# Kernel tuning notes

Measured on AMD Instinct MI355X. Metric: run time of the kernel, lower is better.

## Reference

```python
import jax, jax.numpy as jnp
import numpy as np

H = 4
HD = 32
C = 128
NU = 40000
NI = 40000
E = 200000


def _linear(x, W, b):
    # torch Linear: y = x @ W.T + b, W is [out, in]
    return x @ W.T + b


def _counts_in(query, sorted_keys):
    l = jnp.searchsorted(sorted_keys, query, side='left')
    r = jnp.searchsorted(sorted_keys, query, side='right')
    return (r - l).astype(jnp.float32)


def _segment_softmax(scores, seg, n):
    # scores: [E, H], seg: [E] destination ids
    m = jax.ops.segment_max(scores, seg, num_segments=n)
    m = jnp.where(jnp.isfinite(m), m, 0.0)
    e = jnp.exp(scores - m[seg])
    z = jax.ops.segment_sum(e, seg, num_segments=n)
    return e / z[seg]


def _deg_count(idx, n):
    return jnp.zeros((n,), jnp.float32).at[idx].add(1.0)


def _layernorm(x):
    mu = x.mean(-1, keepdims=True)
    var = ((x - mu) ** 2).mean(-1, keepdims=True)
    return (x - mu) / jnp.sqrt(var + 1e-5)


def _relation(x_src, x_dst, src, dst, t_src, t_dst,
              Wq, bq, Wk, bk, Wv, bv, Wo, bo,
              head_bias, beta, tau_raw, gamma, delta,
              counts, recips, n_dst):
    Q = _linear(x_dst, Wq, bq).reshape(-1, H, HD)
    K = _linear(x_src, Wk, bk).reshape(-1, H, HD)
    V = _linear(x_src, Wv, bv).reshape(-1, H, HD)
    Qe, Ke, Ve = Q[dst], K[src], V[src]                      # [E, H, HD]
    scores = (Qe * Ke).sum(-1) / jnp.sqrt(jnp.float32(HD))   # [E, H]
    scores = scores + head_bias
    dt = jnp.abs(t_dst[dst] - t_src[src]) + 1e-6
    tau = jax.nn.softplus(tau_raw) + 1e-6
    scores = scores + (-jnp.log1p(dt / tau))[:, None] * beta
    scores = scores + jnp.log1p(counts)[:, None] * gamma
    scores = scores + recips[:, None] * delta
    w = _segment_softmax(scores, dst, n_dst)                 # [E, H]
    out_e = (Ve * w[:, :, None]).reshape(-1, C)
    out_e = _linear(out_e, Wo, bo)
    return jnp.zeros((n_dst, C), x_dst.dtype).at[dst].add(out_e)


def setup_inputs() -> dict:
    key = jax.random.key(0)
    ks = jax.random.split(key, 20)
    inp = {
        'x_user': jax.random.normal(ks[0], (NU, C), jnp.float32),
        'x_item': jax.random.normal(ks[1], (NI, C), jnp.float32),
        't_user': jax.random.uniform(ks[2], (NU,), jnp.float32) * 100.0,
        't_item': jax.random.uniform(ks[3], (NI,), jnp.float32) * 100.0,
        'edge_index_ui': jax.random.randint(ks[4], (2, E), 0, NU, jnp.int32),
        'edge_index_iu': jax.random.randint(ks[5], (2, E), 0, NI, jnp.int32),
        'Wq': jax.random.normal(ks[6], (C, C), jnp.float32) * 0.05,
        'bq': jax.random.normal(ks[7], (C,), jnp.float32) * 0.05,
        'Wk': jax.random.normal(ks[8], (C, C), jnp.float32) * 0.05,
        'bk': jax.random.normal(ks[9], (C,), jnp.float32) * 0.05,
        'Wv': jax.random.normal(ks[10], (C, C), jnp.float32) * 0.05,
        'bv': jax.random.normal(ks[11], (C,), jnp.float32) * 0.05,
        'Wo': jax.random.normal(ks[12], (C, C), jnp.float32) * 0.05,
        'bo': jax.random.normal(ks[13], (C,), jnp.float32) * 0.05,
        'rel_head_bias': jax.random.normal(ks[14], (2, H), jnp.float32) * 0.1,
        'time_beta': jax.random.normal(ks[15], (2, H), jnp.float32) * 0.1,
        'time_tau_raw': jax.random.normal(ks[16], (2,), jnp.float32),
        'gamma_multirel': jax.random.normal(ks[17], (2, H), jnp.float32) * 0.1,
        'delta_recip': jax.random.normal(ks[18], (2, H), jnp.float32) * 0.1,
    }
    return inp


def reference(x_user, x_item, t_user, t_item, edge_index_ui, edge_index_iu,
              Wq, bq, Wk, bk, Wv, bv, Wo, bo,
              rel_head_bias, time_beta, time_tau_raw, gamma_multirel, delta_recip):
    su, du = edge_index_ui[0], edge_index_ui[1]   # user -> item
    si, di = edge_index_iu[0], edge_index_iu[1]   # item -> user
    # multirel counts (pair multiplicity - 1) and reciprocity flags, per relation
    pid_ui = su * NI + du            # (user,item) pair ids (fits int32: NU*NI < 2^31)
    pid_iu = si * NU + di            # (item,user) pair ids
    rev_for_ui = di * NI + si        # reversed pairs of iu edges in (user,item) space
    rev_for_iu = du * NU + su        # reversed pairs of ui edges in (item,user) space
    counts_ui = _counts_in(pid_ui, jnp.sort(pid_ui)) - 1.0
    counts_iu = _counts_in(pid_iu, jnp.sort(pid_iu)) - 1.0
    recips_ui = (_counts_in(pid_ui, jnp.sort(rev_for_ui)) > 0).astype(jnp.float32)
    recips_iu = (_counts_in(pid_iu, jnp.sort(rev_for_iu)) > 0).astype(jnp.float32)

    out_item = _relation(x_user, x_item, su, du, t_user, t_item,
                         Wq, bq, Wk, bk, Wv, bv, Wo, bo,
                         rel_head_bias[0], time_beta[0], time_tau_raw[0],
                         gamma_multirel[0], delta_recip[0], counts_ui, recips_ui, NI)
    out_user = _relation(x_item, x_user, si, di, t_item, t_user,
                         Wq, bq, Wk, bk, Wv, bv, Wo, bo,
                         rel_head_bias[1], time_beta[1], time_tau_raw[1],
                         gamma_multirel[1], delta_recip[1], counts_iu, recips_iu, NU)
    # degree centrality bias: total (in + out) degree added to every channel
    deg_user = _deg_count(su, NU) + _deg_count(di, NU)
    deg_item = _deg_count(du, NI) + _deg_count(si, NI)
    out_user = out_user + deg_user[:, None]
    out_item = out_item + deg_item[:, None]
    return _layernorm(out_user + x_user), _layernorm(out_item + x_item)
```

## Files before the change

### kernel.cpp

```cpp
#include <hip/hip_runtime.h>
#include <math.h>

constexpr int kH  = 4;
constexpr int kHD = 32;
constexpr int kC  = 128;
constexpr int kNU = 40000;
constexpr int kNI = 40000;
constexpr int kE  = 200000;
constexpr int kNT = kNU + kNI;
constexpr int kTS = 1 << 19;
constexpr int kTMASK = kTS - 1;
constexpr int kSB = (kNT + 1023) / 1024;
constexpr int kTilesPerSide = kNU / 16;
constexpr int kTiles = kNT / 16;

#define DEV_INLINE __device__ __forceinline__

typedef short bf16x8 __attribute__((ext_vector_type(8)));
typedef float f32x4  __attribute__((ext_vector_type(4)));
typedef uint32_t u32x4 __attribute__((ext_vector_type(4)));

DEV_INLINE int hash_slot(int pid) {
  uint32_t h = (uint32_t)pid * 2654435761u;
  return (int)((h >> 13) & kTMASK);
}

DEV_INLINE unsigned short f2bf(float f) {
  uint32_t u = __float_as_uint(f);
  u += 0x7fffu + ((u >> 16) & 1u);
  return (unsigned short)(u >> 16);
}

DEV_INLINE float bflo(uint32_t u) { return __uint_as_float(u << 16); }
DEV_INLINE float bfhi(uint32_t u) { return __uint_as_float(u & 0xffff0000u); }

DEV_INLINE int swz(int row, int elem) {
  return (elem & 7) | (((elem >> 3) ^ (row & 7)) << 3);
}

__global__ void cast4w_bf16(const float* __restrict__ w0, const float* __restrict__ w1,
                            const float* __restrict__ w2, const float* __restrict__ w3,
                            unsigned short* __restrict__ o0, unsigned short* __restrict__ o1,
                            unsigned short* __restrict__ o2, unsigned short* __restrict__ o3) {
  int i = blockIdx.x * blockDim.x + threadIdx.x;
  int m = i >> 12, j = i & 4095;
  const float* in = (m == 0) ? w0 : (m == 1) ? w1 : (m == 2) ? w2 : w3;
  unsigned short* out = (m == 0) ? o0 : (m == 1) ? o1 : (m == 2) ? o2 : o3;
  float4 v = ((const float4*)in)[j];
  ushort4 o = {f2bf(v.x), f2bf(v.y), f2bf(v.z), f2bf(v.w)};
  ((ushort4*)out)[j] = o;
}

__global__ __launch_bounds__(256, 3) void qkv_ws(
    const float* __restrict__ Xu, const float* __restrict__ Xi,
    const unsigned short* __restrict__ Wq, const unsigned short* __restrict__ Wk,
    const unsigned short* __restrict__ Wv,
    const float* __restrict__ bq, const float* __restrict__ bk,
    const float* __restrict__ bv,
    unsigned short* __restrict__ Qu, unsigned short* __restrict__ Ku,
    unsigned short* __restrict__ Vu,
    unsigned short* __restrict__ Qi, unsigned short* __restrict__ Ki,
    unsigned short* __restrict__ Vi) {
  __shared__ unsigned short sx[16 * kC];
  __shared__ unsigned short sr[3 * 16 * kC];
  const int tid  = threadIdx.x;
  const int wave = tid >> 6;
  const int lane = tid & 63;
  const int mr   = lane & 15;
  const int quad = lane >> 4;
  const int ct0  = wave * 2;
  const int srow = tid >> 4;
  const int schk = tid & 15;

  bf16x8 wf[3][2][4];
  {
    const unsigned short* Ws[3] = {Wq, Wk, Wv};
#pragma unroll
    for (int m = 0; m < 3; ++m)
#pragma unroll
      for (int c = 0; c < 2; ++c) {
        const unsigned short* wrow = Ws[m] + (size_t)((ct0 + c) * 16 + mr) * kC + quad * 8;
#pragma unroll
        for (int kc = 0; kc < 4; ++kc) wf[m][c][kc] = *(const bf16x8*)(wrow + kc * 32);
      }
  }

  int tile = blockIdx.x;
  float4 xa, xb;
  {
    const bool item = tile >= kTilesPerSide;
    const float* X = item ? Xi : Xu;
    const int base = (item ? tile - kTilesPerSide : tile) * 16;
    const float* xr = X + (size_t)(base + srow) * kC + schk * 8;
    xa = ((const float4*)xr)[0];
    xb = ((const float4*)xr)[1];
  }

  for (; tile < kTiles; tile += gridDim.x) {
    const bool item = tile >= kTilesPerSide;
    const int base = (item ? tile - kTilesPerSide : tile) * 16;

    {
      bf16x8 p;
      p[0] = (short)f2bf(xa.x); p[1] = (short)f2bf(xa.y);
      p[2] = (short)f2bf(xa.z); p[3] = (short)f2bf(xa.w);
      p[4] = (short)f2bf(xb.x); p[5] = (short)f2bf(xb.y);
      p[6] = (short)f2bf(xb.z); p[7] = (short)f2bf(xb.w);
      *(bf16x8*)(sx + srow * kC + ((schk ^ (srow & 7)) << 3)) = p;
    }
    __syncthreads();

    bf16x8 b[4];
#pragma unroll
    for (int kc = 0; kc < 4; ++kc)
      b[kc] = *(const bf16x8*)(sx + mr * kC + (((quad + kc * 4) ^ (mr & 7)) << 3));

    int ntile = tile + gridDim.x;
    if (ntile < kTiles) {
      const bool nit = ntile >= kTilesPerSide;
      const float* X = nit ? Xi : Xu;
      const int nbase = (nit ? ntile - kTilesPerSide : ntile) * 16;
      const float* xr = X + (size_t)(nbase + srow) * kC + schk * 8;
      xa = ((const float4*)xr)[0];
      xb = ((const float4*)xr)[1];
    }

    f32x4 acc[3][2];
#pragma unroll
    for (int m = 0; m < 3; ++m) {
      acc[m][0] = (f32x4){0.f, 0.f, 0.f, 0.f};
      acc[m][1] = (f32x4){0.f, 0.f, 0.f, 0.f};
    }
#pragma unroll
    for (int kc = 0; kc < 4; ++kc)
#pragma unroll
      for (int m = 0; m < 3; ++m)
#pragma unroll
        for (int c = 0; c < 2; ++c)
          acc[m][c] = __builtin_amdgcn_mfma_f32_16x16x32_bf16(wf[m][c][kc], b[kc], acc[m][c], 0, 0, 0);

    const float* bs[3] = {bq, bk, bv};
#pragma unroll
    for (int m = 0; m < 3; ++m)
#pragma unroll
      for (int c = 0; c < 2; ++c) {
        int c0 = (ct0 + c) * 16 + quad * 4;
        float4 bb = *(const float4*)(bs[m] + c0);
        uint2 p;
        p.x = (uint32_t)f2bf(acc[m][c][0] + bb.x) | ((uint32_t)f2bf(acc[m][c][1] + bb.y) << 16);
        p.y = (uint32_t)f2bf(acc[m][c][2] + bb.z) | ((uint32_t)f2bf(acc[m][c][3] + bb.w) << 16);
        *(uint2*)(sr + (m * 16 + mr) * kC + swz(mr, c0)) = p;
      }
    __syncthreads();

    {
      unsigned short* Os[3] = {item ? Qi : Qu, item ? Ki : Ku, item ? Vi : Vu};
      const int el = (schk ^ (srow & 7)) << 3;
#pragma unroll
      for (int m = 0; m < 3; ++m) {
        bf16x8 v = *(const bf16x8*)(sr + (m * 16 + srow) * kC + el);
        *(bf16x8*)(Os[m] + (size_t)(base + srow) * kC + schk * 8) = v;
      }
    }
  }
}

DEV_INLINE void table_insert(int* __restrict__ keys, int* __restrict__ cnt, int pid) {
  int slot = hash_slot(pid);
  for (;;) {
    int old = atomicCAS(&keys[slot], -1, pid);
    if (old == -1 || old == pid) { atomicAdd(&cnt[slot], 1); break; }
    slot = (slot + 1) & kTMASK;
  }
}

__global__ void build_table_both(const int* __restrict__ su, const int* __restrict__ du,
                                 const int* __restrict__ si, const int* __restrict__ di,
                                 int* __restrict__ keyA, int* __restrict__ cntA,
                                 int* __restrict__ keyB, int* __restrict__ cntB,
                                 int* __restrict__ deg_all) {
  int t = blockIdx.x * blockDim.x + threadIdx.x;
  if (t >= 2 * kE) return;
  if (t < kE) {
    int s = su[t], d = du[t];
    table_insert(keyA, cntA, s * kNI + d);
    atomicAdd(&deg_all[d], 1);
  } else {
    int e = t - kE;
    int s = si[e], d = di[e];
    table_insert(keyB, cntB, s * kNU + d);
    atomicAdd(&deg_all[kNI + d], 1);
  }
}

DEV_INLINE int table_count(const int* __restrict__ keys, const int* __restrict__ cnt, int pid) {
  int slot = hash_slot(pid);
  for (;;) {
    int k = keys[slot];
    if (k == pid) return cnt[slot];
    if (k == -1) return 0;
    slot = (slot + 1) & kTMASK;
  }
}

__global__ __launch_bounds__(256) void scan1(const int* __restrict__ in,
                                             int* __restrict__ out,
                                             int* __restrict__ bsum, int n) {
  __shared__ int sh[256];
  const int t = threadIdx.x;
  const int base = blockIdx.x * 1024 + t * 4;
  int4 v = {0, 0, 0, 0};
  if (base + 3 < n) {
    v = *(const int4*)(in + base);
  } else {
    if (base + 0 < n) v.x = in[base + 0];
    if (base + 1 < n) v.y = in[base + 1];
    if (base + 2 < n) v.z = in[base + 2];
    if (base + 3 < n) v.w = in[base + 3];
  }
  int s = v.x + v.y + v.z + v.w;
  sh[t] = s;
  __syncthreads();
  int val = s;
  for (int off = 1; off < 256; off <<= 1) {
    int add = (t >= off) ? sh[t - off] : 0;
    __syncthreads();
    val += add;
    sh[t] = val;
    __syncthreads();
  }
  int excl = val - s;
  if (base + 0 < n) out[base + 0] = excl;
  if (base + 1 < n) out[base + 1] = excl + v.x;
  if (base + 2 < n) out[base + 2] = excl + v.x + v.y;
  if (base + 3 < n) out[base + 3] = excl + v.x + v.y + v.z;
  if (t == 255) bsum[blockIdx.x] = val;
}

__global__ __launch_bounds__(128) void scan2(const int* __restrict__ bsum,
                                             int* __restrict__ boff,
                                             int* __restrict__ out_total, int nb) {
  __shared__ int sh[128];
  const int t = threadIdx.x;
  int v = (t < nb) ? bsum[t] : 0;
  sh[t] = v;
  __syncthreads();
  int val = v;
  for (int off = 1; off < 128; off <<= 1) {
    int add = (t >= off) ? sh[t - off] : 0;
    __syncthreads();
    val += add;
    sh[t] = val;
    __syncthreads();
  }
  if (t < nb) boff[t] = val - v;
  if (t == nb - 1) *out_total = val;
}

__global__ __launch_bounds__(256) void scan3(int* __restrict__ out,
                                             const int* __restrict__ boff, int n) {
  const int base = blockIdx.x * 1024 + threadIdx.x * 4;
  const int off = boff[blockIdx.x];
#pragma unroll
  for (int i = 0; i < 4; ++i)
    if (base + i < n) out[base + i] += off;
}

__global__ void scatter_both(const int* __restrict__ du, const int* __restrict__ di,
                             const int* __restrict__ rp_all,
                             int* __restrict__ cur_all, int* __restrict__ el_all) {
  int t = blockIdx.x * blockDim.x + threadIdx.x;
  if (t >= 2 * kE) return;
  if (t < kE) {
    int d = du[t];
    int pos = atomicAdd(&cur_all[d], 1);
    el_all[rp_all[d] + pos] = t;
  } else {
    int e = t - kE;
    int d = di[e];
    int pos = atomicAdd(&cur_all[kNI + d], 1);
    el_all[rp_all[kNI + d] + pos] = e;
  }
}

__global__ void edge_bias_both(const int* __restrict__ su, const int* __restrict__ du,
                               const int* __restrict__ si, const int* __restrict__ di,
                               const float* __restrict__ t_user, const float* __restrict__ t_item,
                               const int* __restrict__ keyA, const int* __restrict__ cntA,
                               const int* __restrict__ keyB, const int* __restrict__ cntB,
                               const float* __restrict__ hb, const float* __restrict__ beta,
                               const float* __restrict__ taur,
                               const float* __restrict__ gamma, const float* __restrict__ delta,
                               float4* __restrict__ bias_ui, float4* __restrict__ bias_iu) {
  int t = blockIdx.x * blockDim.x + threadIdx.x;
  if (t >= 2 * kE) return;
  const int rel = (t >= kE) ? 1 : 0;
  const int e = rel ? t - kE : t;
  int s, d; float ts, td;
  const int *kc_, *cc_, *kr_, *cr_;
  int mulC, mulR;
  if (rel == 0) {
    s = su[e]; d = du[e]; ts = t_user[s]; td = t_item[d];
    kc_ = keyA; cc_ = cntA; mulC = kNI;
    kr_ = keyB; cr_ = cntB; mulR = kNU;
  } else {
    s = si[e]; d = di[e]; ts = t_item[s]; td = t_user[d];
    kc_ = keyB; cc_ = cntB; mulC = kNU;
    kr_ = keyA; cr_ = cntA; mulR = kNI;
  }
  float cntv = (float)(table_count(kc_, cc_, s * mulC + d) - 1);
  float rec  = table_count(kr_, cr_, d * mulR + s) > 0 ? 1.0f : 0.0f;
  float dt   = fabsf(td - ts) + 1e-6f;
  float tau  = log1pf(expf(taur[rel])) + 1e-6f;
  float tterm = -log1pf(dt / tau);
  float lc    = log1pf(cntv);
  const float* hp = hb + rel * kH;
  const float* bp = beta + rel * kH;
  const float* gp = gamma + rel * kH;
  const float* dp = delta + rel * kH;
  const float kL2E = 1.4426950408889634f;
  float4 b;
  b.x = (hp[0] + bp[0] * tterm + gp[0] * lc + dp[0] * rec) * kL2E;
  b.y = (hp[1] + bp[1] * tterm + gp[1] * lc + dp[1] * rec) * kL2E;
  b.z = (hp[2] + bp[2] * tterm + gp[2] * lc + dp[2] * rec) * kL2E;
  b.w = (hp[3] + bp[3] * tterm + gp[3] * lc + dp[3] * rec) * kL2E;
  (rel ? bias_iu : bias_ui)[e] = b;
}

__global__ __launch_bounds__(256) void attn_agg(
    const int* __restrict__ rp_all, const int* __restrict__ el_all,
    const int* __restrict__ su, const int* __restrict__ si,
    const unsigned short* __restrict__ Qi, const unsigned short* __restrict__ Ku,
    const unsigned short* __restrict__ Vu,
    const unsigned short* __restrict__ Qu, const unsigned short* __restrict__ Ki,
    const unsigned short* __restrict__ Vi,
    const float* __restrict__ bias_ui, const float* __restrict__ bias_iu,
    unsigned short* __restrict__ h_ui, unsigned short* __restrict__ h_iu) {
  const int wave = threadIdx.x >> 6;
  const int lane = threadIdx.x & 63;
  const int grp  = lane >> 4;
  const int sub  = lane & 15;
  const int h    = sub >> 2;
  const int ch0  = h * kHD + (sub & 3) * 8;
  const int g = blockIdx.x * 4 + wave;
  if (g >= kNT) return;
  const bool isU = g >= kNI;
  const int n = isU ? g - kNI : g;
  const int* rp = rp_all + (isU ? kNI : 0);
  const int* srcA = isU ? si : su;
  const unsigned short* Q = isU ? Qu : Qi;
  const unsigned short* K = isU ? Ki : Ku;
  const unsigned short* V = isU ? Vi : Vu;
  const float* bias = isU ? bias_iu : bias_ui;
  unsigned short* out = isU ? h_iu : h_ui;

  const int beg = rp[n], end = rp[n + 1];
  const float kScaleL2E = 1.4426950408889634f * 0.17677669529663687f;

  float qf[8];
  {
    u32x4 qv = *(const u32x4*)(Q + (size_t)n * kC + ch0);
#pragma unroll
    for (int w = 0; w < 4; ++w) { qf[2 * w] = bflo(qv[w]); qf[2 * w + 1] = bfhi(qv[w]); }
  }

  float z = 0.f;
  float acc[8] = {0.f, 0.f, 0.f, 0.f, 0.f, 0.f, 0.f, 0.f};

  const int p0 = beg + grp;
  int eA = 0, sA = 0;
  if (p0 < end) { eA = el_all[p0]; sA = srcA[eA]; }
  int eB = 0, sB = 0;
  if (p0 + 4 < end) { eB = el_all[p0 + 4]; sB = srcA[eB]; }
  u32x4 kA = *(const u32x4*)(K + (size_t)sA * kC + ch0);
  u32x4 vA = *(const u32x4*)(V + (size_t)sA * kC + ch0);
  float bA = bias[eA * 4 + h];

  for (int p = p0; p < end; p += 4) {
    u32x4 kB = *(const u32x4*)(K + (size_t)sB * kC + ch0);
    u32x4 vB = *(const u32x4*)(V + (size_t)sB * kC + ch0);
    float bB = bias[eB * 4 + h];
    int eC = 0, sC = 0;
    if (p + 8 < end) { eC = el_all[p + 8]; sC = srcA[eC]; }

    float d0 = qf[0] * bflo(kA[0]);
    float d1 = qf[1] * bfhi(kA[0]);
    d0 = fmaf(qf[2], bflo(kA[1]), d0);
    d1 = fmaf(qf[3], bfhi(kA[1]), d1);
    d0 = fmaf(qf[4], bflo(kA[2]), d0);
    d1 = fmaf(qf[5], bfhi(kA[2]), d1);
    d0 = fmaf(qf[6], bflo(kA[3]), d0);
    d1 = fmaf(qf[7], bfhi(kA[3]), d1);
    float dsc = d0 + d1;
    dsc += __shfl_xor(dsc, 1);
    dsc += __shfl_xor(dsc, 2);
    float wgt = __builtin_amdgcn_exp2f(fmaf(dsc, kScaleL2E, bA));
    z += wgt;
#pragma unroll
    for (int w = 0; w < 4; ++w) {
      acc[2 * w]     = fmaf(bflo(vA[w]), wgt, acc[2 * w]);
      acc[2 * w + 1] = fmaf(bfhi(vA[w]), wgt, acc[2 * w + 1]);
    }
    kA = kB; vA = vB; bA = bB; eB = eC; sB = sC;
  }

#pragma unroll
  for (int j = 0; j < 8; ++j) {
    acc[j] += __shfl_xor(acc[j], 16);
    acc[j] += __shfl_xor(acc[j], 32);
  }
  z += __shfl_xor(z, 16);
  z += __shfl_xor(z, 32);

  const float zi = (end > beg) ? 1.0f / z : 0.0f;
  if (grp == 0) {
    bf16x8 o;
#pragma unroll
    for (int j = 0; j < 8; ++j) o[j] = (short)f2bf(acc[j] * zi);
    *(bf16x8*)(out + (size_t)n * kC + ch0) = o;
  }
}

__global__ __launch_bounds__(256, 4) void wo_ln(
    const unsigned short* __restrict__ Hiu, const unsigned short* __restrict__ Hui,
    const unsigned short* __restrict__ Wo,
    const float* __restrict__ Xu, const float* __restrict__ Xi,
    const int* __restrict__ degU, const int* __restrict__ degI,
    const float* __restrict__ bo, float* __restrict__ out) {
  __shared__ unsigned short sh_h[16 * kC];
  __shared__ float sh_p[64 * 2];
  const int tid  = threadIdx.x;
  const int wave = tid >> 6;
  const int lane = tid & 63;
  const int mr   = lane & 15;
  const int quad = lane >> 4;
  const int ct0  = wave * 2;
  const int srow = tid >> 4;
  const int schk = tid & 15;

  bf16x8 wf[2][4];
#pragma unroll
  for (int c = 0; c < 2; ++c) {
    const unsigned short* wrow = Wo + (size_t)((ct0 + c) * 16 + mr) * kC + quad * 8;
#pragma unroll
    for (int kc = 0; kc < 4; ++kc) wf[c][kc] = *(const bf16x8*)(wrow + kc * 32);
  }
  float4 bb[2];
  bb[0] = *(const float4*)(bo + ct0 * 16 + quad * 4);
  bb[1] = *(const float4*)(bo + (ct0 + 1) * 16 + quad * 4);

  int tile = blockIdx.x;
  bf16x8 hv;
  {
    const bool item = tile >= kTilesPerSide;
    const unsigned short* Hs = item ? Hui : Hiu;
    const int base = (item ? tile - kTilesPerSide : tile) * 16;
    hv = *(const bf16x8*)(Hs + (size_t)(base + srow) * kC + schk * 8);
  }

  for (; tile < kTiles; tile += gridDim.x) {
    const bool item = tile >= kTilesPerSide;
    const int base = (item ? tile - kTilesPerSide : tile) * 16;

    *(bf16x8*)(sh_h + srow * kC + ((schk ^ (srow & 7)) << 3)) = hv;
    __syncthreads();

    bf16x8 b[4];
#pragma unroll
    for (int kc = 0; kc < 4; ++kc)
      b[kc] = *(const bf16x8*)(sh_h + mr * kC + (((quad + kc * 4) ^ (mr & 7)) << 3));

    int ntile = tile + gridDim.x;
    if (ntile < kTiles) {
      const bool nit = ntile >= kTilesPerSide;
      const unsigned short* Hs = nit ? Hui : Hiu;
      const int nbase = (nit ? ntile - kTilesPerSide : ntile) * 16;
      hv = *(const bf16x8*)(Hs + (size_t)(nbase + srow) * kC + schk * 8);
    }

    f32x4 acc[2];
    acc[0] = (f32x4){0.f, 0.f, 0.f, 0.f};
    acc[1] = (f32x4){0.f, 0.f, 0.f, 0.f};
#pragma unroll
    for (int kc = 0; kc < 4; ++kc) {
      acc[0] = __builtin_amdgcn_mfma_f32_16x16x32_bf16(wf[0][kc], b[kc], acc[0], 0, 0, 0);
      acc[1] = __builtin_amdgcn_mfma_f32_16x16x32_bf16(wf[1][kc], b[kc], acc[1], 0, 0, 0);
    }

    const int n = base + mr;
    const float* Xs = item ? Xi : Xu;
    const float fdg = (float)(item ? degI[n] : degU[n]);
    float y[8], s1 = 0.f, s2 = 0.f;
#pragma unroll
    for (int c = 0; c < 2; ++c) {
      int c0 = (ct0 + c) * 16 + quad * 4;
      float4 xv = *(const float4*)(Xs + (size_t)n * kC + c0);
      y[c * 4 + 0] = acc[c][0] + xv.x + fdg * bb[c].x;
      y[c * 4 + 1] = acc[c][1] + xv.y + fdg * bb[c].y;
      y[c * 4 + 2] = acc[c][2] + xv.z + fdg * bb[c].z;
      y[c * 4 + 3] = acc[c][3] + xv.w + fdg * bb[c].w;
#pragma unroll
      for (int j = 0; j < 4; ++j) {
        s1 += y[c * 4 + j];
        s2 += y[c * 4 + j] * y[c * 4 + j];
      }
    }
    s1 += __shfl_xor(s1, 16); s2 += __shfl_xor(s2, 16);
    s1 += __shfl_xor(s1, 32); s2 += __shfl_xor(s2, 32);
    if (quad == 0) {
      sh_p[(wave * 16 + mr) * 2]     = s1;
      sh_p[(wave * 16 + mr) * 2 + 1] = s2;
    }
    __syncthreads();
    float t1 = 0.f, t2 = 0.f;
#pragma unroll
    for (int ww = 0; ww < 4; ++ww) {
      t1 += sh_p[(ww * 16 + mr) * 2];
      t2 += sh_p[(ww * 16 + mr) * 2 + 1];
    }
    float mu   = t1 * (1.0f / 128.0f);
    float var  = t2 * (1.0f / 128.0f) - mu * mu;
    float rstd = rsqrtf(fmaxf(var, 0.0f) + 1e-5f);
    float* op = out + (item ? (size_t)kNU * kC : (size_t)0) + (size_t)n * kC;
#pragma unroll
    for (int c = 0; c < 2; ++c) {
      int c0 = (ct0 + c) * 16 + quad * 4;
      float4 o = {(y[c * 4 + 0] - mu) * rstd, (y[c * 4 + 1] - mu) * rstd,
                  (y[c * 4 + 2] - mu) * rstd, (y[c * 4 + 3] - mu) * rstd};
      *(float4*)(op + c0) = o;
    }
  }
}

extern "C" void kernel_launch(void* const* d_in, const int* in_sizes, int n_in,
                              void* d_out, int out_size, void* d_ws, size_t ws_size,
                              hipStream_t stream) {
  const float* x_user = (const float*)d_in[0];
  const float* x_item = (const float*)d_in[1];
  const float* t_user = (const float*)d_in[2];
  const float* t_item = (const float*)d_in[3];
  const int*   eui    = (const int*)d_in[4];
  const int*   eiu    = (const int*)d_in[5];
  const float* Wq = (const float*)d_in[6];
  const float* bq = (const float*)d_in[7];
  const float* Wk = (const float*)d_in[8];
  const float* bk = (const float*)d_in[9];
  const float* Wv = (const float*)d_in[10];
  const float* bv = (const float*)d_in[11];
  const float* Wo = (const float*)d_in[12];
  const float* bo = (const float*)d_in[13];
  const float* hb    = (const float*)d_in[14];
  const float* beta  = (const float*)d_in[15];
  const float* taur  = (const float*)d_in[16];
  const float* gamma = (const float*)d_in[17];
  const float* delta = (const float*)d_in[18];

  const int* su = eui;       const int* du = eui + kE;
  const int* si = eiu;       const int* di = eiu + kE;

  float* w = (float*)d_ws;
  size_t o = 0;
  unsigned short* qu_b = (unsigned short*)(w + o); o += (size_t)kNU * kC / 2;
  unsigned short* ku_b = (unsigned short*)(w + o); o += (size_t)kNU * kC / 2;
  unsigned short* vu_b = (unsigned short*)(w + o); o += (size_t)kNU * kC / 2;
  unsigned short* qi_b = (unsigned short*)(w + o); o += (size_t)kNI * kC / 2;
  unsigned short* ki_b = (unsigned short*)(w + o); o += (size_t)kNI * kC / 2;
  unsigned short* vi_b = (unsigned short*)(w + o); o += (size_t)kNI * kC / 2;
  unsigned short* h_ui = (unsigned short*)(w + o); o += (size_t)kNI * kC / 2;
  unsigned short* h_iu = (unsigned short*)(w + o); o += (size_t)kNU * kC / 2;
  unsigned short* wq_b = (unsigned short*)(w + o); o += kC * kC / 2;
  unsigned short* wk_b = (unsigned short*)(w + o); o += kC * kC / 2;
  unsigned short* wv_b = (unsigned short*)(w + o); o += kC * kC / 2;
  unsigned short* wo_b = (unsigned short*)(w + o); o += kC * kC / 2;
  float* zero_base = w + o;
  int*   cntA = (int*)(w + o); o += kTS;
  int*   cntB = (int*)(w + o); o += kTS;
  int* deg_all  = (int*)(w + o); o += kNT;
  int* cur_all  = (int*)(w + o); o += kNT;
  size_t zero_bytes = (size_t)((w + o) - zero_base) * sizeof(float);
  int* keyA = (int*)(w + o); o += kTS;
  int* keyB = (int*)(w + o); o += kTS;
  size_t key_bytes = (size_t)2 * kTS * sizeof(int);
  float* bias_ui = w + o; o += (size_t)kE * kH;
  float* bias_iu = w + o; o += (size_t)kE * kH;
  int* rp_all = (int*)(w + o); o += kNT + 1;
  int* el_all = (int*)(w + o); o += 2 * kE;
  int* bsum   = (int*)(w + o); o += kSB;
  int* boff   = (int*)(w + o); o += kSB;

  hipMemsetAsync(zero_base, 0, zero_bytes, stream);
  hipMemsetAsync(keyA, 0xFF, key_bytes, stream);

  dim3 b256(256);
  cast4w_bf16<<<(4 * kC * kC / 4) / 256, b256, 0, stream>>>(Wq, Wk, Wv, Wo,
                                                            wq_b, wk_b, wv_b, wo_b);

  qkv_ws<<<768, b256, 0, stream>>>(x_user, x_item, wq_b, wk_b, wv_b, bq, bk, bv,
                                   qu_b, ku_b, vu_b, qi_b, ki_b, vi_b);

  int g2E = (2 * kE + 255) / 256;
  build_table_both<<<g2E, b256, 0, stream>>>(su, du, si, di, keyA, cntA, keyB, cntB, deg_all);

  scan1<<<kSB, b256, 0, stream>>>(deg_all, rp_all, bsum, kNT);
  scan2<<<1, dim3(128), 0, stream>>>(bsum, boff, rp_all + kNT, kSB);
  scan3<<<kSB, b256, 0, stream>>>(rp_all, boff, kNT);

  scatter_both<<<g2E, b256, 0, stream>>>(du, di, rp_all, cur_all, el_all);

  edge_bias_both<<<g2E, b256, 0, stream>>>(su, du, si, di, t_user, t_item,
                                           keyA, cntA, keyB, cntB,
                                           hb, beta, taur, gamma, delta,
                                           (float4*)bias_ui, (float4*)bias_iu);

  attn_agg<<<kNT / 4, b256, 0, stream>>>(rp_all, el_all, su, si,
                                         qi_b, ku_b, vu_b, qu_b, ki_b, vi_b,
                                         bias_ui, bias_iu, h_ui, h_iu);

  wo_ln<<<768, b256, 0, stream>>>(h_iu, h_ui, wo_b, x_user, x_item,
                                  deg_all + kNI, deg_all, bo, (float*)d_out);
}
```

Measured before the change: 310.1 us.

## Fuse hash-table build into QKV GEMM launch and merge scatter with edge bias

The hash-table build and degree counting now run inside the QKV projection launch: two of every three blocks do table inserts and the third does GEMM tiles, so the atomic-bound and compute-bound work overlap. Each pair key and its count are packed into one 64-bit slot, so a lookup reads a single word. The slot position returned by the degree atomic is saved, which removes the separate cursor-atomic scatter kernel; the scatter is folded into the edge-bias kernel. This saves two launches and some atomics, but the wider key table doubles its memset and memory footprint, and the saved positions reuse the h_ui buffer as scratch.

Result: faster. 264.0 us (-14.9%).

```diff
diff --git a/kernel.cpp b/kernel.cpp
--- a/kernel.cpp
+++ b/kernel.cpp
@@ -13,12 +13,16 @@
 constexpr int kSB = (kNT + 1023) / 1024;
 constexpr int kTilesPerSide = kNU / 16;
 constexpr int kTiles = kNT / 16;
+constexpr int kGemmBlocks  = 768;
+constexpr int kTableBlocks = 1536;
+constexpr int kFusedBlocks = 2304;
 
 #define DEV_INLINE __device__ __forceinline__
 
 typedef short bf16x8 __attribute__((ext_vector_type(8)));
 typedef float f32x4  __attribute__((ext_vector_type(4)));
 typedef uint32_t u32x4 __attribute__((ext_vector_type(4)));
+typedef unsigned long long u64;
 
 DEV_INLINE int hash_slot(int pid) {
   uint32_t h = (uint32_t)pid * 2654435761u;
@@ -36,6 +40,32 @@
 
 DEV_INLINE int swz(int row, int elem) {
   return (elem & 7) | (((elem >> 3) ^ (row & 7)) << 3);
+}
+
+constexpr u64 kEmpty64 = ~0ULL;
+
+DEV_INLINE void table_insert64(u64* __restrict__ keys, int pid) {
+  int slot = hash_slot(pid);
+  const u64 want = (u64)(uint32_t)pid | (1ULL << 32);
+  for (;;) {
+    u64 old = atomicCAS(&keys[slot], kEmpty64, want);
+    if (old == kEmpty64) return;
+    if ((uint32_t)old == (uint32_t)pid) {
+      atomicAdd(&keys[slot], 1ULL << 32);
+      return;
+    }
+    slot = (slot + 1) & kTMASK;
+  }
+}
+
+DEV_INLINE int table_count64(const u64* __restrict__ keys, int pid) {
+  int slot = hash_slot(pid);
+  for (;;) {
+    u64 k = keys[slot];
+    if ((uint32_t)k == (uint32_t)pid) return (int)(k >> 32);
+    if (k == kEmpty64) return 0;
+    slot = (slot + 1) & kTMASK;
+  }
 }
 
 __global__ void cast4w_bf16(const float* __restrict__ w0, const float* __restrict__ w1,
@@ -51,7 +81,7 @@
   ((ushort4*)out)[j] = o;
 }
 
-__global__ __launch_bounds__(256, 3) void qkv_ws(
+__global__ __launch_bounds__(256, 3) void qkv_build(
     const float* __restrict__ Xu, const float* __restrict__ Xi,
     const unsigned short* __restrict__ Wq, const unsigned short* __restrict__ Wk,
     const unsigned short* __restrict__ Wv,
@@ -60,10 +90,34 @@
     unsigned short* __restrict__ Qu, unsigned short* __restrict__ Ku,
     unsigned short* __restrict__ Vu,
     unsigned short* __restrict__ Qi, unsigned short* __restrict__ Ki,
-    unsigned short* __restrict__ Vi) {
+    unsigned short* __restrict__ Vi,
+    const int* __restrict__ su, const int* __restrict__ du,
+    const int* __restrict__ si, const int* __restrict__ di,
+    u64* __restrict__ keyA, u64* __restrict__ keyB,
+    int* __restrict__ deg_all, int* __restrict__ pos_all) {
   __shared__ unsigned short sx[16 * kC];
   __shared__ unsigned short sr[3 * 16 * kC];
-  const int tid  = threadIdx.x;
+  const int bid = blockIdx.x;
+  const int tid = threadIdx.x;
+
+  if (bid % 3 != 1) {
+    const int tb = (bid / 3) * 2 + ((bid % 3) ? 1 : 0);
+    for (int t = tb * 256 + tid; t < 2 * kE; t += kTableBlocks * 256) {
+      if (t < kE) {
+        int s = su[t], d = du[t];
+        table_insert64(keyA, s * kNI + d);
+        pos_all[t] = atomicAdd(&deg_all[d], 1);
+      } else {
+        int e = t - kE;
+        int s = si[e], d = di[e];
+        table_insert64(keyB, s * kNU + d);
+        pos_all[t] = atomicAdd(&deg_all[kNI + d], 1);
+      }
+    }
+    return;
+  }
+
+  const int gb   = bid / 3;
   const int wave = tid >> 6;
   const int lane = tid & 63;
   const int mr   = lane & 15;
@@ -85,7 +139,7 @@
       }
   }
 
-  int tile = blockIdx.x;
+  int tile = gb;
   float4 xa, xb;
   {
     const bool item = tile >= kTilesPerSide;
@@ -96,7 +150,7 @@
     xb = ((const float4*)xr)[1];
   }
 
-  for (; tile < kTiles; tile += gridDim.x) {
+  for (; tile < kTiles; tile += kGemmBlocks) {
     const bool item = tile >= kTilesPerSide;
     const int base = (item ? tile - kTilesPerSide : tile) * 16;
 
@@ -115,7 +169,7 @@
     for (int kc = 0; kc < 4; ++kc)
       b[kc] = *(const bf16x8*)(sx + mr * kC + (((quad + kc * 4) ^ (mr & 7)) << 3));
 
-    int ntile = tile + gridDim.x;
+    int ntile = tile + kGemmBlocks;
     if (ntile < kTiles) {
       const bool nit = ntile >= kTilesPerSide;
       const float* X = nit ? Xi : Xu;
@@ -162,44 +216,6 @@
         *(bf16x8*)(Os[m] + (size_t)(base + srow) * kC + schk * 8) = v;
       }
     }
-  }
-}
-
-DEV_INLINE void table_insert(int* __restrict__ keys, int* __restrict__ cnt, int pid) {
-  int slot = hash_slot(pid);
-  for (;;) {
-    int old = atomicCAS(&keys[slot], -1, pid);
-    if (old == -1 || old == pid) { atomicAdd(&cnt[slot], 1); break; }
-    slot = (slot + 1) & kTMASK;
-  }
-}
-
-__global__ void build_table_both(const int* __restrict__ su, const int* __restrict__ du,
-                                 const int* __restrict__ si, const int* __restrict__ di,
-                                 int* __restrict__ keyA, int* __restrict__ cntA,
-                                 int* __restrict__ keyB, int* __restrict__ cntB,
-                                 int* __restrict__ deg_all) {
-  int t = blockIdx.x * blockDim.x + threadIdx.x;
-  if (t >= 2 * kE) return;
-  if (t < kE) {
-    int s = su[t], d = du[t];
-    table_insert(keyA, cntA, s * kNI + d);
-    atomicAdd(&deg_all[d], 1);
-  } else {
-    int e = t - kE;
-    int s = si[e], d = di[e];
-    table_insert(keyB, cntB, s * kNU + d);
-    atomicAdd(&deg_all[kNI + d], 1);
-  }
-}
-
-DEV_INLINE int table_count(const int* __restrict__ keys, const int* __restrict__ cnt, int pid) {
-  int slot = hash_slot(pid);
-  for (;;) {
-    int k = keys[slot];
-    if (k == pid) return cnt[slot];
-    if (k == -1) return 0;
-    slot = (slot + 1) & kTMASK;
   }
 }
 
@@ -266,50 +282,36 @@
     if (base + i < n) out[base + i] += off;
 }
 
-__global__ void scatter_both(const int* __restrict__ du, const int* __restrict__ di,
-                             const int* __restrict__ rp_all,
-                             int* __restrict__ cur_all, int* __restrict__ el_all) {
-  int t = blockIdx.x * blockDim.x + threadIdx.x;
-  if (t >= 2 * kE) return;
-  if (t < kE) {
-    int d = du[t];
-    int pos = atomicAdd(&cur_all[d], 1);
-    el_all[rp_all[d] + pos] = t;
-  } else {
-    int e = t - kE;
-    int d = di[e];
-    int pos = atomicAdd(&cur_all[kNI + d], 1);
-    el_all[rp_all[kNI + d] + pos] = e;
-  }
-}
-
-__global__ void edge_bias_both(const int* __restrict__ su, const int* __restrict__ du,
-                               const int* __restrict__ si, const int* __restrict__ di,
-                               const float* __restrict__ t_user, const float* __restrict__ t_item,
-                               const int* __restrict__ keyA, const int* __restrict__ cntA,
-                               const int* __restrict__ keyB, const int* __restrict__ cntB,
-                               const float* __restrict__ hb, const float* __restrict__ beta,
-                               const float* __restrict__ taur,
-                               const float* __restrict__ gamma, const float* __restrict__ delta,
-                               float4* __restrict__ bias_ui, float4* __restrict__ bias_iu) {
+__global__ void scatter_bias(const int* __restrict__ su, const int* __restrict__ du,
+                             const int* __restrict__ si, const int* __restrict__ di,
+                             const float* __restrict__ t_user, const float* __restrict__ t_item,
+                             const u64* __restrict__ keyA, const u64* __restrict__ keyB,
+                             const int* __restrict__ rp_all, const int* __restrict__ pos_all,
+                             int* __restrict__ el_all,
+                             const float* __restrict__ hb, const float* __restrict__ beta,
+                             const float* __restrict__ taur,
+                             const float* __restrict__ gamma, const float* __restrict__ delta,
+                             float4* __restrict__ bias_ui, float4* __restrict__ bias_iu) {
   int t = blockIdx.x * blockDim.x + threadIdx.x;
   if (t >= 2 * kE) return;
   const int rel = (t >= kE) ? 1 : 0;
   const int e = rel ? t - kE : t;
   int s, d; float ts, td;
-  const int *kc_, *cc_, *kr_, *cr_;
+  const u64 *kc_, *kr_;
   int mulC, mulR;
   if (rel == 0) {
     s = su[e]; d = du[e]; ts = t_user[s]; td = t_item[d];
-    kc_ = keyA; cc_ = cntA; mulC = kNI;
-    kr_ = keyB; cr_ = cntB; mulR = kNU;
+    kc_ = keyA; mulC = kNI;
+    kr_ = keyB; mulR = kNU;
   } else {
     s = si[e]; d = di[e]; ts = t_item[s]; td = t_user[d];
-    kc_ = keyB; cc_ = cntB; mulC = kNU;
-    kr_ = keyA; cr_ = cntA; mulR = kNI;
-  }
-  float cntv = (float)(table_count(kc_, cc_, s * mulC + d) - 1);
-  float rec  = table_count(kr_, cr_, d * mulR + s) > 0 ? 1.0f : 0.0f;
+    kc_ = keyB; mulC = kNU;
+    kr_ = keyA; mulR = kNI;
+  }
+  const int dg = rel ? kNI + d : d;
+  el_all[rp_all[dg] + pos_all[t]] = e;
+  float cntv = (float)(table_count64(kc_, s * mulC + d) - 1);
+  float rec  = table_count64(kr_, d * mulR + s) > 0 ? 1.0f : 0.0f;
   float dt   = fabsf(td - ts) + 1e-6f;
   float tau  = log1pf(expf(taur[rel])) + 1e-6f;
   float tterm = -log1pf(dt / tau);
@@ -573,20 +575,19 @@
   unsigned short* wv_b = (unsigned short*)(w + o); o += kC * kC / 2;
   unsigned short* wo_b = (unsigned short*)(w + o); o += kC * kC / 2;
   float* zero_base = w + o;
-  int*   cntA = (int*)(w + o); o += kTS;
-  int*   cntB = (int*)(w + o); o += kTS;
-  int* deg_all  = (int*)(w + o); o += kNT;
-  int* cur_all  = (int*)(w + o); o += kNT;
+  int* deg_all = (int*)(w + o); o += kNT;
   size_t zero_bytes = (size_t)((w + o) - zero_base) * sizeof(float);
-  int* keyA = (int*)(w + o); o += kTS;
-  int* keyB = (int*)(w + o); o += kTS;
-  size_t key_bytes = (size_t)2 * kTS * sizeof(int);
+  o = (o + 1) & ~(size_t)1;
+  u64* keyA = (u64*)(w + o); o += (size_t)kTS * 2;
+  u64* keyB = (u64*)(w + o); o += (size_t)kTS * 2;
+  size_t key_bytes = (size_t)2 * kTS * sizeof(u64);
   float* bias_ui = w + o; o += (size_t)kE * kH;
   float* bias_iu = w + o; o += (size_t)kE * kH;
-  int* rp_all = (int*)(w + o); o += kNT + 1;
-  int* el_all = (int*)(w + o); o += 2 * kE;
-  int* bsum   = (int*)(w + o); o += kSB;
-  int* boff   = (int*)(w + o); o += kSB;
+  int* rp_all  = (int*)(w + o); o += kNT + 1;
+  int* el_all  = (int*)(w + o); o += 2 * kE;
+  int* bsum    = (int*)(w + o); o += kSB;
+  int* boff    = (int*)(w + o); o += kSB;
+  int* pos_all = (int*)h_ui;
 
   hipMemsetAsync(zero_base, 0, zero_bytes, stream);
   hipMemsetAsync(keyA, 0xFF, key_bytes, stream);
@@ -595,22 +596,20 @@
   cast4w_bf16<<<(4 * kC * kC / 4) / 256, b256, 0, stream>>>(Wq, Wk, Wv, Wo,
                                                             wq_b, wk_b, wv_b, wo_b);
 
-  qkv_ws<<<768, b256, 0, stream>>>(x_user, x_item, wq_b, wk_b, wv_b, bq, bk, bv,
-                                   qu_b, ku_b, vu_b, qi_b, ki_b, vi_b);
-
-  int g2E = (2 * kE + 255) / 256;
-  build_table_both<<<g2E, b256, 0, stream>>>(su, du, si, di, keyA, cntA, keyB, cntB, deg_all);
+  qkv_build<<<kFusedBlocks, b256, 0, stream>>>(
+      x_user, x_item, wq_b, wk_b, wv_b, bq, bk, bv,
+      qu_b, ku_b, vu_b, qi_b, ki_b, vi_b,
+      su, du, si, di, keyA, keyB, deg_all, pos_all);
 
   scan1<<<kSB, b256, 0, stream>>>(deg_all, rp_all, bsum, kNT);
   scan2<<<1, dim3(128), 0, stream>>>(bsum, boff, rp_all + kNT, kSB);
   scan3<<<kSB, b256, 0, stream>>>(rp_all, boff, kNT);
 
-  scatter_both<<<g2E, b256, 0, stream>>>(du, di, rp_all, cur_all, el_all);
-
-  edge_bias_both<<<g2E, b256, 0, stream>>>(su, du, si, di, t_user, t_item,
-                                           keyA, cntA, keyB, cntB,
-                                           hb, beta, taur, gamma, delta,
-                                           (float4*)bias_ui, (float4*)bias_iu);
+  int g2E = (2 * kE + 255) / 256;
+  scatter_bias<<<g2E, b256, 0, stream>>>(su, du, si, di, t_user, t_item,
+                                         keyA, keyB, rp_all, pos_all, el_all,
+                                         hb, beta, taur, gamma, delta,
+                                         (float4*)bias_ui, (float4*)bias_iu);
 
   attn_agg<<<kNT / 4, b256, 0, stream>>>(rp_all, el_all, su, si,
                                          qi_b, ku_b, vu_b, qu_b, ki_b, vi_b,
```
